# Performance work log

Hardware: AMD Instinct MI355X
Metric: run time of the kernel (lower is better)

## Reference

```python
import jax, jax.numpy as jnp
import numpy as np
import math

B, T, M, C = 4, 2048, 16, 256   # batch, seq, m chunks, c_s chunk width
DIM = 1024                       # layer width; k = DIM // C = 4
D = 64                           # conditioning bottleneck
N_ITERS, TAU = 20, 1.0


def _diag_bias(rows, cols):
    b = np.full((rows, cols), -8.0, dtype=np.float32)
    for i in range(min(rows, cols)):
        b[i, i] = 0.0
    return jnp.asarray(b)


def setup_inputs() -> dict:
    key = jax.random.key(0)
    ks = jax.random.split(key, 10)
    state_dim = M * C
    k = DIM // C
    H_post = np.full((M, k), -8.0, dtype=np.float32)
    for i in range(M):
        H_post[i, i % k] = 0.0
    return {
        "s": jax.random.normal(ks[0], (B, T, M, C), jnp.float32),
        "gamma": 0.02 * jax.random.normal(ks[1], (state_dim,), jnp.float32),
        "compress": 0.02 * jax.random.normal(ks[2], (state_dim, D), jnp.float32),
        "alpha_pre": jnp.float32(0.01),
        "to_logits_pre": 0.02 * jax.random.normal(ks[3], (D, k * M), jnp.float32),
        "H_pre": _diag_bias(k, M),
        "alpha_align": jnp.float32(0.01),
        "to_logits_align": 0.02 * jax.random.normal(ks[4], (D, M * M), jnp.float32),
        "H_align": _diag_bias(M, M),
        "alpha_next": jnp.float32(0.01),
        "to_logits_next": 0.02 * jax.random.normal(ks[5], (D, M * M), jnp.float32),
        "H_next": _diag_bias(M, M),
        "alpha_post": jnp.float32(0.01),
        "to_logits_post": 0.02 * jax.random.normal(ks[6], (D, M * k), jnp.float32),
        "H_post": jnp.asarray(H_post),
        "W_layer": jax.random.normal(ks[7], (DIM, DIM), jnp.float32) / math.sqrt(DIM),
    }


def sinkhorn_log(logits, num_iters=N_ITERS, tau=TAU):
    """Log-domain Sinkhorn; output row-scaled so row sums = 1 * rows-normalized."""
    rows, cols = logits.shape[-2], logits.shape[-1]
    Z = logits / tau
    lr = -math.log(rows)
    lc = -math.log(cols)
    u0 = jnp.zeros(Z.shape[:-1], Z.dtype)
    v0 = jnp.zeros(Z.shape[:-2] + (cols,), Z.dtype)

    def body(_, uv):
        u, v = uv
        u = lr - jax.nn.logsumexp(Z + v[..., None, :], axis=-1)
        v = lc - jax.nn.logsumexp(Z + u[..., None], axis=-2)
        return (u, v)

    u, v = jax.lax.fori_loop(0, num_iters, body, (u0, v0))
    return jnp.exp(Z + u[..., None] + v[..., None, :]) * rows


def _route(code, alpha, to_logits, bias, state, rows, cols):
    """Fused: Sinkhorn(alpha*(code@to_logits)+bias) @ state."""
    raw = (code @ to_logits).reshape(code.shape[:-1] + (rows, cols))
    P = sinkhorn_log(alpha * raw + bias)
    return jnp.einsum('...ij,...jc->...ic', P, state)


def reference(s, gamma, compress, alpha_pre, to_logits_pre, H_pre,
              alpha_align, to_logits_align, H_align,
              alpha_next, to_logits_next, H_next,
              alpha_post, to_logits_post, H_post, W_layer):
    b, t, m, c = s.shape
    state_dim = m * c
    k = W_layer.shape[0] // c
    # RMSNorm over flattened state: F.normalize * sqrt(dim) * (gamma + 1)
    s_vec = s.reshape(b, t, state_dim)
    l2 = jnp.sqrt(jnp.sum(s_vec * s_vec, axis=-1, keepdims=True))
    s_norm = s_vec / jnp.maximum(l2, 1e-12) * jnp.sqrt(jnp.float32(state_dim)) * (gamma + 1.0)
    code = s_norm @ compress  # (b, t, d)
    # read: H_pre (k x m) routes state -> layer input
    layer_in = _route(code, alpha_pre, to_logits_pre, H_pre, s, k, m).reshape(b, t, k * c)
    layer_out = layer_in @ W_layer  # the wrapped layer_fn (dense linear)
    # write: align, absorb output via H_post, prepare next via H_next
    s_aligned = _route(code, alpha_align, to_logits_align, H_align, s, m, m)
    out_flat = layer_out.reshape(b, t, k, c)
    s_updated = s_aligned + _route(code, alpha_post, to_logits_post, H_post, out_flat, m, k)
    s_next = _route(code, alpha_next, to_logits_next, H_next, s_updated, m, m)
    return s_next
```

## Files before the change

kernel.cpp:

```cpp
#include <hip/hip_runtime.h>
#include <math.h>

#define NTOK 8192
#define SD   4096
#define ITERS 20

typedef __attribute__((ext_vector_type(8))) short short8;
typedef __attribute__((ext_vector_type(8))) unsigned short ushort8;
typedef __attribute__((ext_vector_type(4))) unsigned short us4;
typedef __attribute__((ext_vector_type(4))) float f32x4;

__device__ inline unsigned short f2bf(float x) {
    unsigned int u = __float_as_uint(x);
    unsigned int r = (u + 0x7FFFu + ((u >> 16) & 1u)) >> 16;
    return (unsigned short)r;
}
__device__ inline float bf2f(unsigned short u) {
    return __uint_as_float((unsigned int)u << 16);
}

__global__ __launch_bounds__(256) void k_preall(const float* __restrict__ W, unsigned short* __restrict__ WT,
                                                const float* __restrict__ compress, const float* __restrict__ gamma,
                                                unsigned short* __restrict__ cgT,
                                                const float* __restrict__ tl_pre, const float* __restrict__ tl_al,
                                                const float* __restrict__ tl_nx,  const float* __restrict__ tl_po,
                                                unsigned short* __restrict__ tlT)
{
    const int b = blockIdx.x;
    const int tid = threadIdx.x;
    if (b < 256) {
        __shared__ float tb[64][65];
        const int k0 = (b >> 4) * 64, n0 = (b & 15) * 64;
        #pragma unroll 4
        for (int q = 0; q < 16; ++q) {
            const int idx = q * 256 + tid;
            const int r = idx >> 6, c = idx & 63;
            tb[r][c] = W[(size_t)(k0 + r) * 1024 + n0 + c];
        }
        __syncthreads();
        #pragma unroll 4
        for (int q = 0; q < 16; ++q) {
            const int idx = q * 256 + tid;
            const int n = idx >> 6, k = idx & 63;
            WT[(size_t)(n0 + n) * 1024 + k0 + k] = f2bf(tb[k][n]);
        }
    } else if (b < 320) {
        __shared__ float tb2[64][65];
        __shared__ float gsh[64];
        const int k0 = (b - 256) * 64;
        #pragma unroll 4
        for (int q = 0; q < 16; ++q) {
            const int idx = q * 256 + tid;
            const int r = idx >> 6, dd = idx & 63;
            tb2[r][dd] = compress[(size_t)(k0 + r) * 64 + dd];
        }
        if (tid < 64) gsh[tid] = gamma[k0 + tid] + 1.0f;
        __syncthreads();
        #pragma unroll 4
        for (int q = 0; q < 16; ++q) {
            const int idx = q * 256 + tid;
            const int d = idx >> 6, r = idx & 63;
            cgT[(size_t)d * SD + k0 + r] = f2bf(tb2[r][d] * gsh[r]);
        }
    } else {
        const int idx = (b - 320) * 256 + tid;
        const int k = idx / 640, n = idx - k * 640;
        float v;
        if (n < 64)       v = tl_pre[k * 64 + n];
        else if (n < 320) v = tl_al[k * 256 + (n - 64)];
        else if (n < 576) v = tl_nx[k * 256 + (n - 320)];
        else              v = tl_po[k * 64 + (n - 576)];
        tlT[(size_t)n * 64 + k] = f2bf(v);
    }
}

__global__ __launch_bounds__(256) void k_code5(const float* __restrict__ s,
                                               const unsigned short* __restrict__ cgT,
                                               float* __restrict__ code_part,
                                               float* __restrict__ ssq_part)
{
    __shared__ float red[4 * 16 * 68];
    __shared__ float ssq_lds[64];
    const int tid  = threadIdx.x;
    const int lane = tid & 63;
    const int wid  = tid >> 6;
    const int q    = blockIdx.x;
    const int tok0 = blockIdx.y * 16;
    const int row  = lane & 15;
    const int kq   = lane >> 4;
    const int wk   = wid * 32;
    const int kbase = q * 1024;

    float ssq = 0.f;
    f32x4 acc[4];
    #pragma unroll
    for (int ni = 0; ni < 4; ++ni) acc[ni] = (f32x4){0.f, 0.f, 0.f, 0.f};

    const float*          srow  = s   + (size_t)(tok0 + row) * SD + kbase + wk + kq * 8;
    const unsigned short* cgrow = cgT + kbase + wk + kq * 8;

    #pragma unroll
    for (int ks = 0; ks < 8; ++ks) {
        const int kg = ks * 128;
        float4 v0 = *(const float4*)(srow + kg);
        float4 v1 = *(const float4*)(srow + kg + 4);
        ssq += v0.x*v0.x + v0.y*v0.y + v0.z*v0.z + v0.w*v0.w
             + v1.x*v1.x + v1.y*v1.y + v1.z*v1.z + v1.w*v1.w;
        short8 a;
        a[0]=(short)f2bf(v0.x); a[1]=(short)f2bf(v0.y); a[2]=(short)f2bf(v0.z); a[3]=(short)f2bf(v0.w);
        a[4]=(short)f2bf(v1.x); a[5]=(short)f2bf(v1.y); a[6]=(short)f2bf(v1.z); a[7]=(short)f2bf(v1.w);
        short8 b[4];
        #pragma unroll
        for (int ni = 0; ni < 4; ++ni)
            b[ni] = *(const short8*)(cgrow + (size_t)(ni * 16 + row) * SD + kg);
        #pragma unroll
        for (int ni = 0; ni < 4; ++ni)
            acc[ni] = __builtin_amdgcn_mfma_f32_16x16x32_bf16(a, b[ni], acc[ni], 0, 0, 0);
    }

    ssq += __shfl_xor(ssq, 16);
    ssq += __shfl_xor(ssq, 32);
    if (lane < 16) ssq_lds[wid * 16 + row] = ssq;

    #pragma unroll
    for (int ni = 0; ni < 4; ++ni)
        #pragma unroll
        for (int r = 0; r < 4; ++r)
            red[wid * 1088 + ((lane >> 4) * 4 + r) * 68 + ni * 16 + (lane & 15)] = acc[ni][r];
    __syncthreads();
    if (tid < 16)
        ssq_part[(size_t)q * NTOK + tok0 + tid] =
            ssq_lds[tid] + ssq_lds[16 + tid] + ssq_lds[32 + tid] + ssq_lds[48 + tid];
    #pragma unroll
    for (int q2 = 0; q2 < 4; ++q2) {
        const int idx = q2 * 256 + tid;
        const int tok = idx >> 6, d = idx & 63;
        float v = red[0 * 1088 + tok * 68 + d] + red[1 * 1088 + tok * 68 + d]
                + red[2 * 1088 + tok * 68 + d] + red[3 * 1088 + tok * 68 + d];
        code_part[((size_t)q * NTOK + tok0 + tok) * 64 + d] = v;
    }
}

#define LGS 660
__global__ __launch_bounds__(256) void k_sink4(const float* __restrict__ s,
                                               const float* __restrict__ code_part,
                                               const float* __restrict__ ssq_part,
                                               const unsigned short* __restrict__ tlT,
                                               const float* __restrict__ a_pre_p, const float* __restrict__ H_pre,
                                               const float* __restrict__ a_al_p,  const float* __restrict__ H_al,
                                               const float* __restrict__ a_nx_p,  const float* __restrict__ H_nx,
                                               const float* __restrict__ a_po_p,  const float* __restrict__ H_po,
                                               unsigned short* __restrict__ layer_in,
                                               float* __restrict__ Pna, float* __restrict__ Pnp)
{
    __shared__ __align__(16) char smem[48576];
    unsigned short* code_sh = (unsigned short*)(smem);
    unsigned short* lg_sh   = (unsigned short*)(smem + 2304);
    float*          Pnx_sh  = (float*)(smem + 2304);
    float*          Pal_sh  = (float*)(smem + 23424);
    float*          Ppo_sh  = (float*)(smem + 40064);
    float*          ssq_sh  = (float*)(smem + 44416);
    float*          Ppre_sh = (float*)(smem + 44480);

    const int tid  = threadIdx.x;
    const int lane = tid & 63;
    const int wid  = tid >> 6;
    const int tok0 = blockIdx.x * 16;

    float cv[4];
    #pragma unroll
    for (int q2 = 0; q2 < 4; ++q2) {
        const int idx = q2 * 256 + tid;
        const size_t off = (size_t)(tok0 + (idx >> 6)) * 64 + (idx & 63);
        cv[q2] = code_part[off] + code_part[(size_t)NTOK * 64 + off]
               + code_part[(size_t)2 * NTOK * 64 + off] + code_part[(size_t)3 * NTOK * 64 + off];
    }
    if (tid < 16) {
        float t = ssq_part[tok0 + tid] + ssq_part[NTOK + tok0 + tid]
                + ssq_part[2 * NTOK + tok0 + tid] + ssq_part[3 * NTOK + tok0 + tid];
        ssq_sh[tid] = 64.0f / fmaxf(sqrtf(t), 1e-12f);
    }
    __syncthreads();
    #pragma unroll
    for (int q2 = 0; q2 < 4; ++q2) {
        const int idx = q2 * 256 + tid;
        code_sh[(idx >> 6) * 72 + (idx & 63)] = f2bf(cv[q2] * ssq_sh[idx >> 6]);
    }
    __syncthreads();

    {
        f32x4 acc2[10];
        #pragma unroll
        for (int ni = 0; ni < 10; ++ni) acc2[ni] = (f32x4){0.f, 0.f, 0.f, 0.f};
        const int nbase = wid * 160;
        #pragma unroll
        for (int ks = 0; ks < 2; ++ks) {
            const int ko = ks * 32 + (lane >> 4) * 8;
            short8 a = *(const short8*)(code_sh + (lane & 15) * 72 + ko);
            #pragma unroll
            for (int ni = 0; ni < 10; ++ni) {
                short8 b = *(const short8*)(tlT + (size_t)(nbase + ni * 16 + (lane & 15)) * 64 + ko);
                acc2[ni] = __builtin_amdgcn_mfma_f32_16x16x32_bf16(a, b, acc2[ni], 0, 0, 0);
            }
        }
        #pragma unroll
        for (int ni = 0; ni < 10; ++ni)
            #pragma unroll
            for (int r = 0; r < 4; ++r)
                lg_sh[((lane >> 4) * 4 + r) * LGS + nbase + ni * 16 + (lane & 15)] = f2bf(acc2[ni][r]);
    }
    __syncthreads();

    const int t_in = lane >> 2;
    const int sub  = lane & 3;
    float Km[4][16];

    if (wid < 2) {
        const unsigned short* lgp = lg_sh + t_in * LGS + (wid == 0 ? 64 : 320) + sub * 64;
        #pragma unroll
        for (int rr = 0; rr < 4; ++rr)
            #pragma unroll
            for (int h = 0; h < 2; ++h) {
                ushort8 rv = *(const ushort8*)(lgp + rr * 16 + h * 8);
                #pragma unroll
                for (int e = 0; e < 8; ++e) Km[rr][h * 8 + e] = bf2f(rv[e]);
            }
    } else if (wid == 2) {
        const unsigned short* lgp = lg_sh + t_in * LGS + sub * 16;
        #pragma unroll
        for (int h = 0; h < 2; ++h) {
            ushort8 rv = *(const ushort8*)(lgp + h * 8);
            #pragma unroll
            for (int e = 0; e < 8; ++e) Km[0][h * 8 + e] = bf2f(rv[e]);
        }
    } else {
        const unsigned short* lgp = lg_sh + t_in * LGS + 576 + sub * 16;
        #pragma unroll
        for (int rr = 0; rr < 4; ++rr) {
            us4 rv = *(const us4*)(lgp + rr * 4);
            #pragma unroll
            for (int e = 0; e < 4; ++e) Km[rr][e] = bf2f(rv[e]);
        }
    }
    __syncthreads();

    if (wid < 2) {
        const float alpha = (wid == 0) ? (*a_al_p) : (*a_nx_p);
        const float* Hp   = ((wid == 0) ? H_al : H_nx) + sub * 64;
        #pragma unroll
        for (int rr = 0; rr < 4; ++rr)
            #pragma unroll
            for (int c = 0; c < 16; ++c)
                Km[rr][c] = __expf(alpha * Km[rr][c] + Hp[rr * 16 + c]);
        float v[16], u[4];
        #pragma unroll
        for (int c = 0; c < 16; ++c) v[c] = 1.0f;
        for (int it = 0; it < ITERS; ++it) {
            #pragma unroll
            for (int rr = 0; rr < 4; ++rr) {
                float su = 0.f;
                #pragma unroll
                for (int c = 0; c < 16; ++c) su += Km[rr][c] * v[c];
                u[rr] = 0.0625f * __builtin_amdgcn_rcpf(su);
            }
            float pv[16];
            #pragma unroll
            for (int c = 0; c < 16; ++c)
                pv[c] = Km[0][c]*u[0] + Km[1][c]*u[1] + Km[2][c]*u[2] + Km[3][c]*u[3];
            #pragma unroll
            for (int c = 0; c < 16; ++c) pv[c] += __shfl_xor(pv[c], 1);
            #pragma unroll
            for (int c = 0; c < 16; ++c) pv[c] += __shfl_xor(pv[c], 2);
            #pragma unroll
            for (int c = 0; c < 16; ++c) v[c] = 0.0625f * __builtin_amdgcn_rcpf(pv[c]);
        }
        float* dst = ((wid == 0) ? Pal_sh : Pnx_sh) + t_in * 260;
        #pragma unroll
        for (int rr = 0; rr < 4; ++rr) {
            const float su16 = 16.0f * u[rr];
            #pragma unroll
            for (int c = 0; c < 16; ++c)
                dst[(sub * 4 + rr) * 16 + c] = Km[rr][c] * su16 * v[c];
        }
    } else if (wid == 2) {
        const float alpha = *a_pre_p;
        const float* Hp  = H_pre + sub * 16;
        #pragma unroll
        for (int c = 0; c < 16; ++c) Km[0][c] = __expf(alpha * Km[0][c] + Hp[c]);
        float v[16], u;
        #pragma unroll
        for (int c = 0; c < 16; ++c) v[c] = 1.0f;
        for (int it = 0; it < ITERS; ++it) {
            float su = 0.f;
            #pragma unroll
            for (int c = 0; c < 16; ++c) su += Km[0][c] * v[c];
            u = 0.25f * __builtin_amdgcn_rcpf(su);
            float pv[16];
            #pragma unroll
            for (int c = 0; c < 16; ++c) pv[c] = Km[0][c] * u;
            #pragma unroll
            for (int c = 0; c < 16; ++c) pv[c] += __shfl_xor(pv[c], 1);
            #pragma unroll
            for (int c = 0; c < 16; ++c) pv[c] += __shfl_xor(pv[c], 2);
            #pragma unroll
            for (int c = 0; c < 16; ++c) v[c] = 0.0625f * __builtin_amdgcn_rcpf(pv[c]);
        }
        const float su4 = 4.0f * u;
        #pragma unroll
        for (int c = 0; c < 16; ++c)
            Ppre_sh[t_in * 64 + sub * 16 + c] = Km[0][c] * su4 * v[c];
    } else {
        const float alpha = *a_po_p;
        const float* Hp  = H_po + sub * 16;
        #pragma unroll
        for (int rr = 0; rr < 4; ++rr)
            #pragma unroll
            for (int c = 0; c < 4; ++c)
                Km[rr][c] = __expf(alpha * Km[rr][c] + Hp[rr * 4 + c]);
        float v[4], u[4];
        #pragma unroll
        for (int c = 0; c < 4; ++c) v[c] = 1.0f;
        for (int it = 0; it < ITERS; ++it) {
            #pragma unroll
            for (int rr = 0; rr < 4; ++rr) {
                float su = 0.f;
                #pragma unroll
                for (int c = 0; c < 4; ++c) su += Km[rr][c] * v[c];
                u[rr] = 0.0625f * __builtin_amdgcn_rcpf(su);
            }
            float pv[4];
            #pragma unroll
            for (int c = 0; c < 4; ++c)
                pv[c] = Km[0][c]*u[0] + Km[1][c]*u[1] + Km[2][c]*u[2] + Km[3][c]*u[3];
            #pragma unroll
            for (int c = 0; c < 4; ++c) pv[c] += __shfl_xor(pv[c], 1);
            #pragma unroll
            for (int c = 0; c < 4; ++c) pv[c] += __shfl_xor(pv[c], 2);
            #pragma unroll
            for (int c = 0; c < 4; ++c) v[c] = 0.25f * __builtin_amdgcn_rcpf(pv[c]);
        }
        #pragma unroll
        for (int rr = 0; rr < 4; ++rr) {
            const float su16 = 16.0f * u[rr];
            #pragma unroll
            for (int c = 0; c < 4; ++c)
                Ppo_sh[t_in * 68 + (sub * 4 + rr) * 4 + c] = Km[rr][c] * su16 * v[c];
        }
    }
    __syncthreads();

    const int ct = tid >> 4;
    const int cj = tid & 15;
    const float* pnx = Pnx_sh + ct * 260;
    const float* pal = Pal_sh + ct * 260;
    const float* ppo = Ppo_sh + ct * 68;
    #pragma unroll
    for (int m = 0; m < 16; ++m) {
        float a2 = 0.f;
        #pragma unroll
        for (int t2 = 0; t2 < 16; ++t2) a2 += pnx[m * 16 + t2] * pal[t2 * 16 + cj];
        Pna[(size_t)(tok0 + ct) * 256 + m * 16 + cj] = a2;
    }
    #pragma unroll
    for (int e = 0; e < 4; ++e) {
        const int idx = cj * 4 + e;
        const int m = idx >> 2, q = idx & 3;
        float a2 = 0.f;
        #pragma unroll
        for (int t2 = 0; t2 < 16; ++t2) a2 += pnx[m * 16 + t2] * ppo[t2 * 4 + q];
        Pnp[(size_t)(tok0 + ct) * 64 + idx] = a2;
    }

    const float* sblk = s + (size_t)tok0 * SD;
    #pragma unroll 2
    for (int t = 0; t < 16; ++t) {
        const float* srow2 = sblk + (size_t)t * SD + tid;
        float sv[16];
        #pragma unroll
        for (int j = 0; j < 16; ++j) sv[j] = srow2[j * 256];
        const float* pp = Ppre_sh + t * 64;
        unsigned short* lo = layer_in + (size_t)(tok0 + t) * 1024 + tid;
        #pragma unroll
        for (int i = 0; i < 4; ++i) {
            float a3 = 0.f;
            #pragma unroll
            for (int j = 0; j < 16; ++j) a3 += pp[i * 16 + j] * sv[j];
            lo[i * 256] = f2bf(a3);
        }
    }
}

__global__ __launch_bounds__(256) void k_gemm_bf16(const unsigned short* __restrict__ A,
                                                   const unsigned short* __restrict__ BT,
                                                   unsigned short* __restrict__ Cb)
{
    __shared__ unsigned short Abuf[128 * 48];
    __shared__ unsigned short Bbuf[128 * 48];
    const int tid  = threadIdx.x;
    const int lane = tid & 63;
    const int wid  = tid >> 6;
    const int wr   = wid >> 1, wc = wid & 1;
    const int m0 = blockIdx.y * 128, n0 = blockIdx.x * 128;

    f32x4 acc[4][4];
    #pragma unroll
    for (int mi = 0; mi < 4; ++mi)
        #pragma unroll
        for (int ni = 0; ni < 4; ++ni) acc[mi][ni] = (f32x4){0.f, 0.f, 0.f, 0.f};

    for (int k0 = 0; k0 < 1024; k0 += 32) {
        __syncthreads();
        #pragma unroll
        for (int h = 0; h < 2; ++h) {
            const int idx = h * 256 + tid;
            const int row = idx >> 2, kq = idx & 3;
            float4 av = *(const float4*)(A + (size_t)(m0 + row) * 1024 + k0 + kq * 8);
            *(float4*)(Abuf + row * 48 + kq * 8) = av;
            float4 bv = *(const float4*)(BT + (size_t)(n0 + row) * 1024 + k0 + kq * 8);
            *(float4*)(Bbuf + row * 48 + kq * 8) = bv;
        }
        __syncthreads();

        short8 a[4], b[4];
        #pragma unroll
        for (int mi = 0; mi < 4; ++mi)
            a[mi] = *(const short8*)(Abuf + (wr * 64 + mi * 16 + (lane & 15)) * 48 + (lane >> 4) * 8);
        #pragma unroll
        for (int ni = 0; ni < 4; ++ni)
            b[ni] = *(const short8*)(Bbuf + (wc * 64 + ni * 16 + (lane & 15)) * 48 + (lane >> 4) * 8);
        #pragma unroll
        for (int mi = 0; mi < 4; ++mi)
            #pragma unroll
            for (int ni = 0; ni < 4; ++ni)
                acc[mi][ni] = __builtin_amdgcn_mfma_f32_16x16x32_bf16(a[mi], b[ni], acc[mi][ni], 0, 0, 0);
    }

    #pragma unroll
    for (int mi = 0; mi < 4; ++mi)
        #pragma unroll
        for (int ni = 0; ni < 4; ++ni)
            #pragma unroll
            for (int r = 0; r < 4; ++r)
                Cb[(size_t)(m0 + wr * 64 + mi * 16 + (lane >> 4) * 4 + r) * 1024 +
                   n0 + wc * 64 + ni * 16 + (lane & 15)] = f2bf(acc[mi][ni][r]);
}

__global__ __launch_bounds__(256) void k_final(const float* __restrict__ s,
                                               const unsigned short* __restrict__ lo_bf,
                                               const float* __restrict__ Pna,
                                               const float* __restrict__ Pnp,
                                               float* __restrict__ out)
{
    __shared__ float s_sh[SD];
    __shared__ float lo_sh[1024];
    __shared__ float Pna_sh[256];
    __shared__ float Pnp_sh[64];
    const int tid = threadIdx.x;
    const int tok = blockIdx.x;

    {
        const float4* sp4 = (const float4*)(s + (size_t)tok * SD);
        #pragma unroll
        for (int j = 0; j < 4; ++j)
            *(float4*)(s_sh + j * 1024 + tid * 4) = sp4[j * 256 + tid];
    }
    {
        us4 lv = *(const us4*)(lo_bf + (size_t)tok * 1024 + tid * 4);
        float4 f;
        f.x = bf2f(lv[0]); f.y = bf2f(lv[1]); f.z = bf2f(lv[2]); f.w = bf2f(lv[3]);
        *(float4*)(lo_sh + tid * 4) = f;
    }
    Pna_sh[tid] = Pna[(size_t)tok * 256 + tid];
    if (tid < 64) Pnp_sh[tid] = Pnp[(size_t)tok * 64 + tid];
    __syncthreads();

    const int c = tid;
    #pragma unroll
    for (int m = 0; m < 16; ++m) {
        float acc = 0.f;
        #pragma unroll
        for (int j = 0; j < 16; ++j) acc += Pna_sh[m * 16 + j] * s_sh[j * 256 + c];
        #pragma unroll
        for (int q = 0; q < 4; ++q) acc += Pnp_sh[m * 4 + q] * lo_sh[q * 256 + c];
        out[(size_t)tok * SD + m * 256 + c] = acc;
    }
}

extern "C" void kernel_launch(void* const* d_in, const int* in_sizes, int n_in,
                              void* d_out, int out_size, void* d_ws, size_t ws_size,
                              hipStream_t stream)
{
    const float* s        = (const float*)d_in[0];
    const float* gamma    = (const float*)d_in[1];
    const float* compress = (const float*)d_in[2];
    const float* a_pre    = (const float*)d_in[3];
    const float* tl_pre   = (const float*)d_in[4];
    const float* H_pre    = (const float*)d_in[5];
    const float* a_al     = (const float*)d_in[6];
    const float* tl_al    = (const float*)d_in[7];
    const float* H_al     = (const float*)d_in[8];
    const float* a_nx     = (const float*)d_in[9];
    const float* tl_nx    = (const float*)d_in[10];
    const float* H_nx     = (const float*)d_in[11];
    const float* a_po     = (const float*)d_in[12];
    const float* tl_po    = (const float*)d_in[13];
    const float* H_po     = (const float*)d_in[14];
    const float* W        = (const float*)d_in[15];
    float* out = (float*)d_out;

    char* p = (char*)d_ws;
    unsigned short* lo_bf    = (unsigned short*)p; p += (size_t)8192 * 1024 * 2;
    float* Pna               = (float*)p;          p += (size_t)8192 * 256 * 4;
    float* Pnp               = (float*)p;          p += (size_t)8192 * 64 * 4;
    unsigned short* layer_in = (unsigned short*)p; p += (size_t)8192 * 1024 * 2;
    unsigned short* WT       = (unsigned short*)p; p += (size_t)1024 * 1024 * 2;
    unsigned short* cgT      = (unsigned short*)p; p += (size_t)64 * SD * 2;
    unsigned short* tlT      = (unsigned short*)p; p += (size_t)640 * 64 * 2 + 128;
    float* code_part         = (float*)p;          p += (size_t)4 * NTOK * 64 * 4;
    float* ssq_part          = (float*)p;          p += (size_t)4 * NTOK * 4;

    k_preall<<<480, 256, 0, stream>>>(W, WT, compress, gamma, cgT,
                                      tl_pre, tl_al, tl_nx, tl_po, tlT);
    k_code5<<<dim3(4, 512), 256, 0, stream>>>(s, cgT, code_part, ssq_part);
    k_sink4<<<512, 256, 0, stream>>>(s, code_part, ssq_part, tlT,
                                     a_pre, H_pre, a_al, H_al,
                                     a_nx, H_nx, a_po, H_po,
                                     layer_in, Pna, Pnp);
    k_gemm_bf16<<<dim3(8, 64), 256, 0, stream>>>(layer_in, WT, lo_bf);
    k_final<<<NTOK, 256, 0, stream>>>(s, lo_bf, Pna, Pnp, out);
}
```

Measured before the change: 188.5 us.

## Halve tokens per block in sinkhorn kernel and vectorize layer_in routing loads

The sinkhorn/routing kernel now handles 8 tokens per block instead of 16. The grid doubles to 1024 blocks and shared memory shrinks to about 25KB, which raises occupancy and spreads the serial 20-iteration Sinkhorn loops across more CUs. In exchange, half the lanes in each wave sit idle during the Sinkhorn phase, and MFMA rows beyond 8 are computed on zero padding and discarded. The final pre-routing step now reads s with float4 loads and writes four bf16 outputs per store, which should improve memory coalescing.

```diff
diff --git a/kernel.cpp b/kernel.cpp
--- a/kernel.cpp
+++ b/kernel.cpp
@@ -142,47 +142,48 @@
 }
 
 #define LGS 660
-__global__ __launch_bounds__(256) void k_sink4(const float* __restrict__ s,
-                                               const float* __restrict__ code_part,
-                                               const float* __restrict__ ssq_part,
-                                               const unsigned short* __restrict__ tlT,
-                                               const float* __restrict__ a_pre_p, const float* __restrict__ H_pre,
-                                               const float* __restrict__ a_al_p,  const float* __restrict__ H_al,
-                                               const float* __restrict__ a_nx_p,  const float* __restrict__ H_nx,
-                                               const float* __restrict__ a_po_p,  const float* __restrict__ H_po,
-                                               unsigned short* __restrict__ layer_in,
-                                               float* __restrict__ Pna, float* __restrict__ Pnp)
+__global__ __launch_bounds__(256) void k_sink4b(const float* __restrict__ s,
+                                                const float* __restrict__ code_part,
+                                                const float* __restrict__ ssq_part,
+                                                const unsigned short* __restrict__ tlT,
+                                                const float* __restrict__ a_pre_p, const float* __restrict__ H_pre,
+                                                const float* __restrict__ a_al_p,  const float* __restrict__ H_al,
+                                                const float* __restrict__ a_nx_p,  const float* __restrict__ H_nx,
+                                                const float* __restrict__ a_po_p,  const float* __restrict__ H_po,
+                                                unsigned short* __restrict__ layer_in,
+                                                float* __restrict__ Pna, float* __restrict__ Pnp)
 {
-    __shared__ __align__(16) char smem[48576];
+    __shared__ __align__(16) char smem[25472];
     unsigned short* code_sh = (unsigned short*)(smem);
     unsigned short* lg_sh   = (unsigned short*)(smem + 2304);
     float*          Pnx_sh  = (float*)(smem + 2304);
-    float*          Pal_sh  = (float*)(smem + 23424);
-    float*          Ppo_sh  = (float*)(smem + 40064);
-    float*          ssq_sh  = (float*)(smem + 44416);
-    float*          Ppre_sh = (float*)(smem + 44480);
+    float*          Pal_sh  = (float*)(smem + 12864);
+    float*          Ppo_sh  = (float*)(smem + 21184);
+    float*          ssq_sh  = (float*)(smem + 23360);
+    float*          Ppre_sh = (float*)(smem + 23392);
 
     const int tid  = threadIdx.x;
     const int lane = tid & 63;
     const int wid  = tid >> 6;
-    const int tok0 = blockIdx.x * 16;
-
-    float cv[4];
-    #pragma unroll
-    for (int q2 = 0; q2 < 4; ++q2) {
+    const int tok0 = blockIdx.x * 8;
+
+    float cv[2];
+    #pragma unroll
+    for (int q2 = 0; q2 < 2; ++q2) {
         const int idx = q2 * 256 + tid;
         const size_t off = (size_t)(tok0 + (idx >> 6)) * 64 + (idx & 63);
         cv[q2] = code_part[off] + code_part[(size_t)NTOK * 64 + off]
                + code_part[(size_t)2 * NTOK * 64 + off] + code_part[(size_t)3 * NTOK * 64 + off];
     }
-    if (tid < 16) {
+    if (tid < 8) {
         float t = ssq_part[tok0 + tid] + ssq_part[NTOK + tok0 + tid]
                 + ssq_part[2 * NTOK + tok0 + tid] + ssq_part[3 * NTOK + tok0 + tid];
         ssq_sh[tid] = 64.0f / fmaxf(sqrtf(t), 1e-12f);
     }
-    __syncthreads();
-    #pragma unroll
-    for (int q2 = 0; q2 < 4; ++q2) {
+    for (int i = 576 + tid; i < 1152; i += 256) code_sh[i] = 0;
+    __syncthreads();
+    #pragma unroll
+    for (int q2 = 0; q2 < 2; ++q2) {
         const int idx = q2 * 256 + tid;
         code_sh[(idx >> 6) * 72 + (idx & 63)] = f2bf(cv[q2] * ssq_sh[idx >> 6]);
     }
@@ -203,189 +204,206 @@
                 acc2[ni] = __builtin_amdgcn_mfma_f32_16x16x32_bf16(a, b, acc2[ni], 0, 0, 0);
             }
         }
-        #pragma unroll
-        for (int ni = 0; ni < 10; ++ni)
-            #pragma unroll
-            for (int r = 0; r < 4; ++r)
-                lg_sh[((lane >> 4) * 4 + r) * LGS + nbase + ni * 16 + (lane & 15)] = f2bf(acc2[ni][r]);
+        const int orow = (lane >> 4) * 4;
+        if (orow < 8) {
+            #pragma unroll
+            for (int ni = 0; ni < 10; ++ni)
+                #pragma unroll
+                for (int r = 0; r < 4; ++r)
+                    lg_sh[(orow + r) * LGS + nbase + ni * 16 + (lane & 15)] = f2bf(acc2[ni][r]);
+        }
     }
     __syncthreads();
 
     const int t_in = lane >> 2;
     const int sub  = lane & 3;
+    const bool act = (t_in < 8);
     float Km[4][16];
 
-    if (wid < 2) {
-        const unsigned short* lgp = lg_sh + t_in * LGS + (wid == 0 ? 64 : 320) + sub * 64;
-        #pragma unroll
-        for (int rr = 0; rr < 4; ++rr)
+    if (act) {
+        if (wid < 2) {
+            const unsigned short* lgp = lg_sh + t_in * LGS + (wid == 0 ? 64 : 320) + sub * 64;
+            #pragma unroll
+            for (int rr = 0; rr < 4; ++rr)
+                #pragma unroll
+                for (int h = 0; h < 2; ++h) {
+                    ushort8 rv = *(const ushort8*)(lgp + rr * 16 + h * 8);
+                    #pragma unroll
+                    for (int e = 0; e < 8; ++e) Km[rr][h * 8 + e] = bf2f(rv[e]);
+                }
+        } else if (wid == 2) {
+            const unsigned short* lgp = lg_sh + t_in * LGS + sub * 16;
             #pragma unroll
             for (int h = 0; h < 2; ++h) {
-                ushort8 rv = *(const ushort8*)(lgp + rr * 16 + h * 8);
-                #pragma unroll
-                for (int e = 0; e < 8; ++e) Km[rr][h * 8 + e] = bf2f(rv[e]);
-            }
-    } else if (wid == 2) {
-        const unsigned short* lgp = lg_sh + t_in * LGS + sub * 16;
-        #pragma unroll
-        for (int h = 0; h < 2; ++h) {
-            ushort8 rv = *(const ushort8*)(lgp + h * 8);
-            #pragma unroll
-            for (int e = 0; e < 8; ++e) Km[0][h * 8 + e] = bf2f(rv[e]);
-        }
-    } else {
-        const unsigned short* lgp = lg_sh + t_in * LGS + 576 + sub * 16;
-        #pragma unroll
-        for (int rr = 0; rr < 4; ++rr) {
-            us4 rv = *(const us4*)(lgp + rr * 4);
-            #pragma unroll
-            for (int e = 0; e < 4; ++e) Km[rr][e] = bf2f(rv[e]);
-        }
-    }
-    __syncthreads();
-
-    if (wid < 2) {
-        const float alpha = (wid == 0) ? (*a_al_p) : (*a_nx_p);
-        const float* Hp   = ((wid == 0) ? H_al : H_nx) + sub * 64;
-        #pragma unroll
-        for (int rr = 0; rr < 4; ++rr)
+                ushort8 rv = *(const ushort8*)(lgp + h * 8);
+                #pragma unroll
+                for (int e = 0; e < 8; ++e) Km[0][h * 8 + e] = bf2f(rv[e]);
+            }
+        } else {
+            const unsigned short* lgp = lg_sh + t_in * LGS + 576 + sub * 16;
+            #pragma unroll
+            for (int rr = 0; rr < 4; ++rr) {
+                us4 rv = *(const us4*)(lgp + rr * 4);
+                #pragma unroll
+                for (int e = 0; e < 4; ++e) Km[rr][e] = bf2f(rv[e]);
+            }
+        }
+    }
+    __syncthreads();
+
+    if (act) {
+        if (wid < 2) {
+            const float alpha = (wid == 0) ? (*a_al_p) : (*a_nx_p);
+            const float* Hp   = ((wid == 0) ? H_al : H_nx) + sub * 64;
+            #pragma unroll
+            for (int rr = 0; rr < 4; ++rr)
+                #pragma unroll
+                for (int c = 0; c < 16; ++c)
+                    Km[rr][c] = __expf(alpha * Km[rr][c] + Hp[rr * 16 + c]);
+            float v[16], u[4];
+            #pragma unroll
+            for (int c = 0; c < 16; ++c) v[c] = 1.0f;
+            for (int it = 0; it < ITERS; ++it) {
+                #pragma unroll
+                for (int rr = 0; rr < 4; ++rr) {
+                    float su = 0.f;
+                    #pragma unroll
+                    for (int c = 0; c < 16; ++c) su += Km[rr][c] * v[c];
+                    u[rr] = 0.0625f * __builtin_amdgcn_rcpf(su);
+                }
+                float pv[16];
+                #pragma unroll
+                for (int c = 0; c < 16; ++c)
+                    pv[c] = Km[0][c]*u[0] + Km[1][c]*u[1] + Km[2][c]*u[2] + Km[3][c]*u[3];
+                #pragma unroll
+                for (int c = 0; c < 16; ++c) pv[c] += __shfl_xor(pv[c], 1);
+                #pragma unroll
+                for (int c = 0; c < 16; ++c) pv[c] += __shfl_xor(pv[c], 2);
+                #pragma unroll
+                for (int c = 0; c < 16; ++c) v[c] = 0.0625f * __builtin_amdgcn_rcpf(pv[c]);
+            }
+            float* dst = ((wid == 0) ? Pal_sh : Pnx_sh) + t_in * 260;
+            #pragma unroll
+            for (int rr = 0; rr < 4; ++rr) {
+                const float su16 = 16.0f * u[rr];
+                #pragma unroll
+                for (int c = 0; c < 16; ++c)
+                    dst[(sub * 4 + rr) * 16 + c] = Km[rr][c] * su16 * v[c];
+            }
+        } else if (wid == 2) {
+            const float alpha = *a_pre_p;
+            const float* Hp  = H_pre + sub * 16;
+            #pragma unroll
+            for (int c = 0; c < 16; ++c) Km[0][c] = __expf(alpha * Km[0][c] + Hp[c]);
+            float v[16], u;
+            #pragma unroll
+            for (int c = 0; c < 16; ++c) v[c] = 1.0f;
+            for (int it = 0; it < ITERS; ++it) {
+                float su = 0.f;
+                #pragma unroll
+                for (int c = 0; c < 16; ++c) su += Km[0][c] * v[c];
+                u = 0.25f * __builtin_amdgcn_rcpf(su);
+                float pv[16];
+                #pragma unroll
+                for (int c = 0; c < 16; ++c) pv[c] = Km[0][c] * u;
+                #pragma unroll
+                for (int c = 0; c < 16; ++c) pv[c] += __shfl_xor(pv[c], 1);
+                #pragma unroll
+                for (int c = 0; c < 16; ++c) pv[c] += __shfl_xor(pv[c], 2);
+                #pragma unroll
+                for (int c = 0; c < 16; ++c) v[c] = 0.0625f * __builtin_amdgcn_rcpf(pv[c]);
+            }
+            const float su4 = 4.0f * u;
             #pragma unroll
             for (int c = 0; c < 16; ++c)
-                Km[rr][c] = __expf(alpha * Km[rr][c] + Hp[rr * 16 + c]);
-        float v[16], u[4];
-        #pragma unroll
-        for (int c = 0; c < 16; ++c) v[c] = 1.0f;
-        for (int it = 0; it < ITERS; ++it) {
+                Ppre_sh[t_in * 64 + sub * 16 + c] = Km[0][c] * su4 * v[c];
+        } else {
+            const float alpha = *a_po_p;
+            const float* Hp  = H_po + sub * 16;
+            #pragma unroll
+            for (int rr = 0; rr < 4; ++rr)
+                #pragma unroll
+                for (int c = 0; c < 4; ++c)
+                    Km[rr][c] = __expf(alpha * Km[rr][c] + Hp[rr * 4 + c]);
+            float v[4], u[4];
+            #pragma unroll
+            for (int c = 0; c < 4; ++c) v[c] = 1.0f;
+            for (int it = 0; it < ITERS; ++it) {
+                #pragma unroll
+                for (int rr = 0; rr < 4; ++rr) {
+                    float su = 0.f;
+                    #pragma unroll
+                    for (int c = 0; c < 4; ++c) su += Km[rr][c] * v[c];
+                    u[rr] = 0.0625f * __builtin_amdgcn_rcpf(su);
+                }
+                float pv[4];
+                #pragma unroll
+                for (int c = 0; c < 4; ++c)
+                    pv[c] = Km[0][c]*u[0] + Km[1][c]*u[1] + Km[2][c]*u[2] + Km[3][c]*u[3];
+                #pragma unroll
+                for (int c = 0; c < 4; ++c) pv[c] += __shfl_xor(pv[c], 1);
+                #pragma unroll
+                for (int c = 0; c < 4; ++c) pv[c] += __shfl_xor(pv[c], 2);
+                #pragma unroll
+                for (int c = 0; c < 4; ++c) v[c] = 0.25f * __builtin_amdgcn_rcpf(pv[c]);
+            }
             #pragma unroll
             for (int rr = 0; rr < 4; ++rr) {
-                float su = 0.f;
-                #pragma unroll
-                for (int c = 0; c < 16; ++c) su += Km[rr][c] * v[c];
-                u[rr] = 0.0625f * __builtin_amdgcn_rcpf(su);
-            }
-            float pv[16];
-            #pragma unroll
-            for (int c = 0; c < 16; ++c)
-                pv[c] = Km[0][c]*u[0] + Km[1][c]*u[1] + Km[2][c]*u[2] + Km[3][c]*u[3];
-            #pragma unroll
-            for (int c = 0; c < 16; ++c) pv[c] += __shfl_xor(pv[c], 1);
-            #pragma unroll
-            for (int c = 0; c < 16; ++c) pv[c] += __shfl_xor(pv[c], 2);
-            #pragma unroll
-            for (int c = 0; c < 16; ++c) v[c] = 0.0625f * __builtin_amdgcn_rcpf(pv[c]);
-        }
-        float* dst = ((wid == 0) ? Pal_sh : Pnx_sh) + t_in * 260;
-        #pragma unroll
-        for (int rr = 0; rr < 4; ++rr) {
-            const float su16 = 16.0f * u[rr];
-            #pragma unroll
-            for (int c = 0; c < 16; ++c)
-                dst[(sub * 4 + rr) * 16 + c] = Km[rr][c] * su16 * v[c];
-        }
-    } else if (wid == 2) {
-        const float alpha = *a_pre_p;
-        const float* Hp  = H_pre + sub * 16;
-        #pragma unroll
-        for (int c = 0; c < 16; ++c) Km[0][c] = __expf(alpha * Km[0][c] + Hp[c]);
-        float v[16], u;
-        #pragma unroll
-        for (int c = 0; c < 16; ++c) v[c] = 1.0f;
-        for (int it = 0; it < ITERS; ++it) {
-            float su = 0.f;
-            #pragma unroll
-            for (int c = 0; c < 16; ++c) su += Km[0][c] * v[c];
-            u = 0.25f * __builtin_amdgcn_rcpf(su);
-            float pv[16];
-            #pragma unroll
-            for (int c = 0; c < 16; ++c) pv[c] = Km[0][c] * u;
-            #pragma unroll
-            for (int c = 0; c < 16; ++c) pv[c] += __shfl_xor(pv[c], 1);
-            #pragma unroll
-            for (int c = 0; c < 16; ++c) pv[c] += __shfl_xor(pv[c], 2);
-            #pragma unroll
-            for (int c = 0; c < 16; ++c) v[c] = 0.0625f * __builtin_amdgcn_rcpf(pv[c]);
-        }
-        const float su4 = 4.0f * u;
-        #pragma unroll
-        for (int c = 0; c < 16; ++c)
-            Ppre_sh[t_in * 64 + sub * 16 + c] = Km[0][c] * su4 * v[c];
-    } else {
-        const float alpha = *a_po_p;
-        const float* Hp  = H_po + sub * 16;
-        #pragma unroll
-        for (int rr = 0; rr < 4; ++rr)
-            #pragma unroll
-            for (int c = 0; c < 4; ++c)
-                Km[rr][c] = __expf(alpha * Km[rr][c] + Hp[rr * 4 + c]);
-        float v[4], u[4];
-        #pragma unroll
-        for (int c = 0; c < 4; ++c) v[c] = 1.0f;
-        for (int it = 0; it < ITERS; ++it) {
-            #pragma unroll
-            for (int rr = 0; rr < 4; ++rr) {
-                float su = 0.f;
-                #pragma unroll
-                for (int c = 0; c < 4; ++c) su += Km[rr][c] * v[c];
-                u[rr] = 0.0625f * __builtin_amdgcn_rcpf(su);
-            }
-            float pv[4];
-            #pragma unroll
-            for (int c = 0; c < 4; ++c)
-                pv[c] = Km[0][c]*u[0] + Km[1][c]*u[1] + Km[2][c]*u[2] + Km[3][c]*u[3];
-            #pragma unroll
-            for (int c = 0; c < 4; ++c) pv[c] += __shfl_xor(pv[c], 1);
-            #pragma unroll
-            for (int c = 0; c < 4; ++c) pv[c] += __shfl_xor(pv[c], 2);
-            #pragma unroll
-            for (int c = 0; c < 4; ++c) v[c] = 0.25f * __builtin_amdgcn_rcpf(pv[c]);
-        }
-        #pragma unroll
-        for (int rr = 0; rr < 4; ++rr) {
-            const float su16 = 16.0f * u[rr];
-            #pragma unroll
-            for (int c = 0; c < 4; ++c)
-                Ppo_sh[t_in * 68 + (sub * 4 + rr) * 4 + c] = Km[rr][c] * su16 * v[c];
+                const float su16 = 16.0f * u[rr];
+                #pragma unroll
+                for (int c = 0; c < 4; ++c)
+                    Ppo_sh[t_in * 68 + (sub * 4 + rr) * 4 + c] = Km[rr][c] * su16 * v[c];
+            }
         }
     }
     __syncthreads();
 
     const int ct = tid >> 4;
     const int cj = tid & 15;
-    const float* pnx = Pnx_sh + ct * 260;
-    const float* pal = Pal_sh + ct * 260;
-    const float* ppo = Ppo_sh + ct * 68;
-    #pragma unroll
-    for (int m = 0; m < 16; ++m) {
-        float a2 = 0.f;
-        #pragma unroll
-        for (int t2 = 0; t2 < 16; ++t2) a2 += pnx[m * 16 + t2] * pal[t2 * 16 + cj];
-        Pna[(size_t)(tok0 + ct) * 256 + m * 16 + cj] = a2;
-    }
-    #pragma unroll
-    for (int e = 0; e < 4; ++e) {
-        const int idx = cj * 4 + e;
-        const int m = idx >> 2, q = idx & 3;
-        float a2 = 0.f;
-        #pragma unroll
-        for (int t2 = 0; t2 < 16; ++t2) a2 += pnx[m * 16 + t2] * ppo[t2 * 4 + q];
-        Pnp[(size_t)(tok0 + ct) * 64 + idx] = a2;
-    }
-
-    const float* sblk = s + (size_t)tok0 * SD;
-    #pragma unroll 2
-    for (int t = 0; t < 16; ++t) {
-        const float* srow2 = sblk + (size_t)t * SD + tid;
-        float sv[16];
-        #pragma unroll
-        for (int j = 0; j < 16; ++j) sv[j] = srow2[j * 256];
+    if (ct < 8) {
+        const float* pnx = Pnx_sh + ct * 260;
+        const float* pal = Pal_sh + ct * 260;
+        const float* ppo = Ppo_sh + ct * 68;
+        #pragma unroll
+        for (int m = 0; m < 16; ++m) {
+            float a2 = 0.f;
+            #pragma unroll
+            for (int t2 = 0; t2 < 16; ++t2) a2 += pnx[m * 16 + t2] * pal[t2 * 16 + cj];
+            Pna[(size_t)(tok0 + ct) * 256 + m * 16 + cj] = a2;
+        }
+        #pragma unroll
+        for (int e = 0; e < 4; ++e) {
+            const int idx = cj * 4 + e;
+            const int m = idx >> 2, q = idx & 3;
+            float a2 = 0.f;
+            #pragma unroll
+            for (int t2 = 0; t2 < 16; ++t2) a2 += pnx[m * 16 + t2] * ppo[t2 * 4 + q];
+            Pnp[(size_t)(tok0 + ct) * 64 + idx] = a2;
+        }
+    }
+
+    #pragma unroll
+    for (int tg = 0; tg < 2; ++tg) {
+        const int t = tg * 4 + (tid >> 6);
+        const int c4 = tid & 63;
+        const float4* sp = (const float4*)(s + (size_t)(tok0 + t) * SD) + c4;
+        float4 sv[16];
+        #pragma unroll
+        for (int j = 0; j < 16; ++j) sv[j] = sp[j * 64];
         const float* pp = Ppre_sh + t * 64;
-        unsigned short* lo = layer_in + (size_t)(tok0 + t) * 1024 + tid;
+        unsigned short* lo = layer_in + (size_t)(tok0 + t) * 1024 + c4 * 4;
         #pragma unroll
         for (int i = 0; i < 4; ++i) {
-            float a3 = 0.f;
-            #pragma unroll
-            for (int j = 0; j < 16; ++j) a3 += pp[i * 16 + j] * sv[j];
-            lo[i * 256] = f2bf(a3);
+            float ax = 0.f, ay = 0.f, az = 0.f, aw = 0.f;
+            #pragma unroll
+            for (int j = 0; j < 16; ++j) {
+                const float pij = pp[i * 16 + j];
+                ax += pij * sv[j].x; ay += pij * sv[j].y;
+                az += pij * sv[j].z; aw += pij * sv[j].w;
+            }
+            us4 o;
+            o[0] = f2bf(ax); o[1] = f2bf(ay); o[2] = f2bf(az); o[3] = f2bf(aw);
+            *(us4*)(lo + i * 256) = o;
         }
     }
 }
@@ -522,10 +540,10 @@
     k_preall<<<480, 256, 0, stream>>>(W, WT, compress, gamma, cgT,
                                       tl_pre, tl_al, tl_nx, tl_po, tlT);
     k_code5<<<dim3(4, 512), 256, 0, stream>>>(s, cgT, code_part, ssq_part);
-    k_sink4<<<512, 256, 0, stream>>>(s, code_part, ssq_part, tlT,
-                                     a_pre, H_pre, a_al, H_al,
-                                     a_nx, H_nx, a_po, H_po,
-                                     layer_in, Pna, Pnp);
+    k_sink4b<<<1024, 256, 0, stream>>>(s, code_part, ssq_part, tlT,
+                                       a_pre, H_pre, a_al, H_al,
+                                       a_nx, H_nx, a_po, H_po,
+                                       layer_in, Pna, Pnp);
     k_gemm_bf16<<<dim3(8, 64), 256, 0, stream>>>(layer_in, WT, lo_bf);
     k_final<<<NTOK, 256, 0, stream>>>(s, lo_bf, Pna, Pnp, out);
 }
```

Result: slower. 205.7 us (+9.1%).
